# Optimization experiments

Measured on AMD Instinct MI355X. Metric: run time of the kernel, lower is better.

## Reference

```python
import jax, jax.numpy as jnp
import numpy as np


def _ste_sign(x):
    # sign with straight-through (identity) gradient, matching gradient_override_map({'Sign': 'Identity'})
    return x + jax.lax.stop_gradient(jnp.sign(x) - x)


def _ternarize(W):
    # threshold = 0.7 * mean(|W|)
    t = 0.7 * jnp.mean(jnp.abs(W))
    # alpha = mean of |W| over entries with |W| strictly beyond threshold
    pos = jnp.where(W > t, W, jnp.zeros_like(W))
    neg = jnp.where(W < -t, W, jnp.zeros_like(W))
    a = jnp.abs(pos + neg)
    n = jnp.sum(jnp.where(a > 0, jnp.ones_like(a), jnp.zeros_like(a)))
    alpha = jnp.sum(a) / n
    # ternary weights in {-1, 0, +1}: sign(sign(W+t) + sign(W-t))
    Wq = _ste_sign(_ste_sign(W + t) + _ste_sign(W - t))
    return alpha * Wq


def setup_inputs() -> dict:
    key = jax.random.key(0)
    kx, kw = jax.random.split(key)
    x = jax.random.normal(kx, (32, 56, 56, 256), dtype=jnp.float32)      # NHWC
    W = jax.random.normal(kw, (3, 3, 256, 256), dtype=jnp.float32) * 0.02  # HWIO, stddev=0.02 init
    b = jnp.zeros((256,), dtype=jnp.float32)
    return {"x": x, "W": W, "b": b}


def reference(x, W, b):
    Wq = _ternarize(W)
    y = jax.lax.conv_general_dilated(
        x, Wq,
        window_strides=(1, 1),
        padding='SAME',
        dimension_numbers=('NHWC', 'HWIO', 'NHWC'),
    )
    return y + b  # act = identity
```

## Files before the change

kernel.cpp:

```cpp
#include <hip/hip_runtime.h>
#include <hip/hip_bf16.h>
#include <stdint.h>


typedef __attribute__((ext_vector_type(8))) short short8;
typedef __attribute__((ext_vector_type(4))) float floatx4;

#define NW_ELEMS 589824
#define K_TOTAL 2304
#define PR_OFF 0
#define QV_OFF 2560
#define QC_OFF 5120
#define WQT_OFF 8192
#define XPAD_OFF 1187840
#define RED_BLOCKS 288
#define PAD_BLOCKS 13456

__device__ __forceinline__ void async16(const void* g, void* l) {
  __builtin_amdgcn_global_load_lds(
      (const __attribute__((address_space(1))) void*)g,
      (__attribute__((address_space(3))) void*)l, 16, 0, 0);
}

__device__ __forceinline__ ushort f2bf(float f) {
  __hip_bfloat16 h = __float2bfloat16(f);
  return *reinterpret_cast<ushort*>(&h);
}

__global__ __launch_bounds__(256) void pad_sumabs_kernel(
    const float* __restrict__ x, ushort* __restrict__ xpad,
    const float* __restrict__ W, double* __restrict__ pr) {
  if (blockIdx.x < RED_BLOCKS) {
    __shared__ double sds[4];
    double v = 0.0;
#pragma unroll
    for (int j = 0; j < 8; j++) {
      uint i = (blockIdx.x * 8 + j) * 256 + threadIdx.x;
      v += (double)fabsf(W[i]);
    }
#pragma unroll
    for (int off = 32; off; off >>= 1) v += __shfl_down(v, off);
    if ((threadIdx.x & 63) == 0) sds[threadIdx.x >> 6] = v;
    __syncthreads();
    if (threadIdx.x == 0) pr[blockIdx.x] = sds[0] + sds[1] + sds[2] + sds[3];
    return;
  }
  uint idx = (blockIdx.x - RED_BLOCKS) * 256 + threadIdx.x;
  uint c8 = idx & 31;
  uint sp = idx >> 5;
  uint ww = sp % 58;
  uint t = sp / 58;
  uint hh = t % 58;
  uint n = t / 58;
  ushort* dst = xpad + ((size_t)sp * 256 + c8 * 8);
  if (hh == 0 || hh == 57 || ww == 0 || ww == 57) {
    uint4 z = {0, 0, 0, 0};
    *(uint4*)dst = z;
  } else {
    const float* src = x + (((size_t)(n * 56 + (hh - 1)) * 56 + (ww - 1)) * 256 + c8 * 8);
    float4 f0 = *(const float4*)src;
    float4 f1 = *(const float4*)(src + 4);
    ushort u[8];
    u[0] = f2bf(f0.x); u[1] = f2bf(f0.y); u[2] = f2bf(f0.z); u[3] = f2bf(f0.w);
    u[4] = f2bf(f1.x); u[5] = f2bf(f1.y); u[6] = f2bf(f1.z); u[7] = f2bf(f1.w);
    *(uint4*)dst = *(uint4*)u;
  }
}

__global__ __launch_bounds__(256) void quant_kernel(
    const float* __restrict__ W, ushort* __restrict__ WqT,
    const double* __restrict__ pr, double* __restrict__ qv,
    unsigned long long* __restrict__ qc) {
  __shared__ double sds[4];
  __shared__ unsigned long long cds[4];
  double p = pr[threadIdx.x];
  if (threadIdx.x < 32) p += pr[256 + threadIdx.x];
#pragma unroll
  for (int off = 32; off; off >>= 1) p += __shfl_down(p, off);
  if ((threadIdx.x & 63) == 0) sds[threadIdx.x >> 6] = p;
  __syncthreads();
  double s = sds[0] + sds[1] + sds[2] + sds[3];
  float t = (float)(0.7 * (s / (double)NW_ELEMS));
  __syncthreads();

  double v = 0.0;
  unsigned long long cnt = 0;
  ushort u[8];
#pragma unroll
  for (int j = 0; j < 8; j++) {
    uint i = (blockIdx.x * 8 + j) * 256 + threadIdx.x;
    float w = W[i];
    bool pos = (w > t), neg = (w < -t);
    u[j] = pos ? (ushort)0x3F80 : (neg ? (ushort)0xBF80 : (ushort)0);
    if (pos || neg) { v += (double)fabsf(w); cnt++; }
  }
  *(uint4*)(WqT + (size_t)threadIdx.x * K_TOTAL + blockIdx.x * 8) = *(uint4*)u;
#pragma unroll
  for (int off = 32; off; off >>= 1) {
    v += __shfl_down(v, off);
    cnt += __shfl_down(cnt, off);
  }
  if ((threadIdx.x & 63) == 0) { sds[threadIdx.x >> 6] = v; cds[threadIdx.x >> 6] = cnt; }
  __syncthreads();
  if (threadIdx.x == 0) {
    qv[blockIdx.x] = sds[0] + sds[1] + sds[2] + sds[3];
    qc[blockIdx.x] = cds[0] + cds[1] + cds[2] + cds[3];
  }
}

__global__ __launch_bounds__(256, 2) void conv_kernel(
    const ushort* __restrict__ xpad, const ushort* __restrict__ WqT,
    const double* __restrict__ qv, const unsigned long long* __restrict__ qc,
    const float* __restrict__ bias, float* __restrict__ out) {
  __shared__ __attribute__((aligned(16))) ushort Alds[128 * 64];
  __shared__ __attribute__((aligned(16))) ushort Blds[128 * 64];
  __shared__ double ads[4];
  __shared__ double acs[4];
  uint tid = threadIdx.x;
  uint bm = blockIdx.x >> 1, bn = blockIdx.x & 1;

  uint chunk = tid & 7;
  uint rbase = tid >> 3;
  uint ceff = chunk ^ (rbase & 7);
  const ushort* asrc[4];
  const ushort* bsrc[4];
#pragma unroll
  for (int i = 0; i < 4; i++) {
    uint row = i * 32 + rbase;
    uint gm = bm * 128 + row;
    uint n = gm / 3136;
    uint rem = gm - n * 3136;
    uint h = rem / 56;
    uint w = rem - h * 56;
    asrc[i] = xpad + (((size_t)(n * 58 + h) * 58 + w) * 256 + ceff * 8);
    bsrc[i] = WqT + ((size_t)(bn * 128 + row) * K_TOTAL + ceff * 8);
  }

  floatx4 acc[4][4];
#pragma unroll
  for (int mt = 0; mt < 4; mt++)
#pragma unroll
    for (int nt = 0; nt < 4; nt++) acc[mt][nt] = (floatx4){0.f, 0.f, 0.f, 0.f};

  uint lane = tid & 63;
  uint wv = tid >> 6;
  uint wm = wv >> 1, wn = wv & 1;
  uint fr = lane & 15, fq = lane >> 4;
  uint a_row = (wm * 64 + fr) * 128;
  uint b_row = (wn * 64 + fr) * 128;
  uint swz = (fr & 7) * 16;

  for (int ks = 0; ks < 36; ks++) {
    uint kcq = (uint)ks / 9;
    uint tap = (uint)ks - kcq * 9;
    uint ky = tap / 3;
    uint kx = tap - ky * 3;
    uint aoffe = (ky * 58 + kx) * 256 + kcq * 64;
    uint boffe = tap * 256 + kcq * 64;

    __syncthreads();
#pragma unroll
    for (int i = 0; i < 4; i++)
      async16(asrc[i] + aoffe, (char*)Alds + i * 4096 + tid * 16);
#pragma unroll
    for (int i = 0; i < 4; i++)
      async16(bsrc[i] + boffe, (char*)Blds + i * 4096 + tid * 16);
    __syncthreads();

#pragma unroll
    for (int kk = 0; kk < 2; kk++) {
      uint csl = ((uint)(kk * 64) + fq * 16) ^ swz;
      short8 af[4], bfr[4];
#pragma unroll
      for (int mt = 0; mt < 4; mt++)
        af[mt] = *(const short8*)((const char*)Alds + a_row + mt * 2048 + csl);
#pragma unroll
      for (int nt = 0; nt < 4; nt++)
        bfr[nt] = *(const short8*)((const char*)Blds + b_row + nt * 2048 + csl);
#pragma unroll
      for (int mt = 0; mt < 4; mt++)
#pragma unroll
        for (int nt = 0; nt < 4; nt++)
          acc[mt][nt] = __builtin_amdgcn_mfma_f32_16x16x32_bf16(
              af[mt], bfr[nt], acc[mt][nt], 0, 0, 0);
    }
  }

  double av = qv[tid];
  double ac = (double)qc[tid];
  if (tid < 32) { av += qv[256 + tid]; ac += (double)qc[256 + tid]; }
#pragma unroll
  for (int off = 32; off; off >>= 1) {
    av += __shfl_down(av, off);
    ac += __shfl_down(ac, off);
  }
  if ((tid & 63) == 0) { ads[tid >> 6] = av; acs[tid >> 6] = ac; }
  __syncthreads();
  float alpha = (float)((ads[0] + ads[1] + ads[2] + ads[3]) /
                        (acs[0] + acs[1] + acs[2] + acs[3]));

#pragma unroll
  for (int mt = 0; mt < 4; mt++) {
    uint mb = bm * 128 + wm * 64 + mt * 16 + fq * 4;
#pragma unroll
    for (int r = 0; r < 4; r++) {
      float* orow = out + (size_t)(mb + r) * 256;
#pragma unroll
      for (int nt = 0; nt < 4; nt++) {
        uint n = bn * 128 + wn * 64 + nt * 16 + fr;
        orow[n] = acc[mt][nt][r] * alpha + bias[n];
      }
    }
  }
}

extern "C" void kernel_launch(void* const* d_in, const int* in_sizes, int n_in,
                              void* d_out, int out_size, void* d_ws, size_t ws_size,
                              hipStream_t stream) {
  const float* x = (const float*)d_in[0];
  const float* W = (const float*)d_in[1];
  const float* b = (const float*)d_in[2];
  float* out = (float*)d_out;

  double* pr = (double*)((char*)d_ws + PR_OFF);
  double* qv = (double*)((char*)d_ws + QV_OFF);
  unsigned long long* qc = (unsigned long long*)((char*)d_ws + QC_OFF);
  ushort* WqT = (ushort*)((char*)d_ws + WQT_OFF);
  ushort* xpad = (ushort*)((char*)d_ws + XPAD_OFF);

  pad_sumabs_kernel<<<RED_BLOCKS + PAD_BLOCKS, 256, 0, stream>>>(x, xpad, W, pr);
  quant_kernel<<<RED_BLOCKS, 256, 0, stream>>>(W, WqT, pr, qv, qc);
  conv_kernel<<<1568, 256, 0, stream>>>(xpad, WqT, qv, qc, b, out);
}
```

Baseline: 294.0 us.

## Fuse padding and bf16 conversion of input into conv kernel A-tile loads

Removes the separate pass that pads the input and writes a bf16 copy. The conv kernel now reads fp32 activations directly, does bounds checks for the halo, converts to bf16 in registers and stores the A tile into LDS with ordinary stores instead of async global-to-LDS loads. This saves a full write and read of the padded activation tensor. In exchange, each activation is read as fp32 (twice the bytes), is re-read and re-converted by every N-block and tap, and the synchronous loads may stall the MFMA loop.

```diff
diff --git a/kernel.cpp b/kernel.cpp
--- a/kernel.cpp
+++ b/kernel.cpp
@@ -12,9 +12,7 @@
 #define QV_OFF 2560
 #define QC_OFF 5120
 #define WQT_OFF 8192
-#define XPAD_OFF 1187840
 #define RED_BLOCKS 288
-#define PAD_BLOCKS 13456
 
 __device__ __forceinline__ void async16(const void* g, void* l) {
   __builtin_amdgcn_global_load_lds(
@@ -27,44 +25,20 @@
   return *reinterpret_cast<ushort*>(&h);
 }
 
-__global__ __launch_bounds__(256) void pad_sumabs_kernel(
-    const float* __restrict__ x, ushort* __restrict__ xpad,
+__global__ __launch_bounds__(256) void sumabs_kernel(
     const float* __restrict__ W, double* __restrict__ pr) {
-  if (blockIdx.x < RED_BLOCKS) {
-    __shared__ double sds[4];
-    double v = 0.0;
-#pragma unroll
-    for (int j = 0; j < 8; j++) {
-      uint i = (blockIdx.x * 8 + j) * 256 + threadIdx.x;
-      v += (double)fabsf(W[i]);
-    }
-#pragma unroll
-    for (int off = 32; off; off >>= 1) v += __shfl_down(v, off);
-    if ((threadIdx.x & 63) == 0) sds[threadIdx.x >> 6] = v;
-    __syncthreads();
-    if (threadIdx.x == 0) pr[blockIdx.x] = sds[0] + sds[1] + sds[2] + sds[3];
-    return;
-  }
-  uint idx = (blockIdx.x - RED_BLOCKS) * 256 + threadIdx.x;
-  uint c8 = idx & 31;
-  uint sp = idx >> 5;
-  uint ww = sp % 58;
-  uint t = sp / 58;
-  uint hh = t % 58;
-  uint n = t / 58;
-  ushort* dst = xpad + ((size_t)sp * 256 + c8 * 8);
-  if (hh == 0 || hh == 57 || ww == 0 || ww == 57) {
-    uint4 z = {0, 0, 0, 0};
-    *(uint4*)dst = z;
-  } else {
-    const float* src = x + (((size_t)(n * 56 + (hh - 1)) * 56 + (ww - 1)) * 256 + c8 * 8);
-    float4 f0 = *(const float4*)src;
-    float4 f1 = *(const float4*)(src + 4);
-    ushort u[8];
-    u[0] = f2bf(f0.x); u[1] = f2bf(f0.y); u[2] = f2bf(f0.z); u[3] = f2bf(f0.w);
-    u[4] = f2bf(f1.x); u[5] = f2bf(f1.y); u[6] = f2bf(f1.z); u[7] = f2bf(f1.w);
-    *(uint4*)dst = *(uint4*)u;
-  }
+  __shared__ double sds[4];
+  double v = 0.0;
+#pragma unroll
+  for (int j = 0; j < 8; j++) {
+    uint i = (blockIdx.x * 8 + j) * 256 + threadIdx.x;
+    v += (double)fabsf(W[i]);
+  }
+#pragma unroll
+  for (int off = 32; off; off >>= 1) v += __shfl_down(v, off);
+  if ((threadIdx.x & 63) == 0) sds[threadIdx.x >> 6] = v;
+  __syncthreads();
+  if (threadIdx.x == 0) pr[blockIdx.x] = sds[0] + sds[1] + sds[2] + sds[3];
 }
 
 __global__ __launch_bounds__(256) void quant_kernel(
@@ -109,7 +83,7 @@
 }
 
 __global__ __launch_bounds__(256, 2) void conv_kernel(
-    const ushort* __restrict__ xpad, const ushort* __restrict__ WqT,
+    const float* __restrict__ x, const ushort* __restrict__ WqT,
     const double* __restrict__ qv, const unsigned long long* __restrict__ qc,
     const float* __restrict__ bias, float* __restrict__ out) {
   __shared__ __attribute__((aligned(16))) ushort Alds[128 * 64];
@@ -122,7 +96,8 @@
   uint chunk = tid & 7;
   uint rbase = tid >> 3;
   uint ceff = chunk ^ (rbase & 7);
-  const ushort* asrc[4];
+  int hh[4], ww[4];
+  int abase[4];
   const ushort* bsrc[4];
 #pragma unroll
   for (int i = 0; i < 4; i++) {
@@ -132,7 +107,9 @@
     uint rem = gm - n * 3136;
     uint h = rem / 56;
     uint w = rem - h * 56;
-    asrc[i] = xpad + (((size_t)(n * 58 + h) * 58 + w) * 256 + ceff * 8);
+    hh[i] = (int)h;
+    ww[i] = (int)w;
+    abase[i] = (((int)n * 56 + (int)h - 1) * 56 + (int)w - 1) * 256 + (int)(ceff * 8);
     bsrc[i] = WqT + ((size_t)(bn * 128 + row) * K_TOTAL + ceff * 8);
   }
 
@@ -153,18 +130,31 @@
   for (int ks = 0; ks < 36; ks++) {
     uint kcq = (uint)ks / 9;
     uint tap = (uint)ks - kcq * 9;
-    uint ky = tap / 3;
-    uint kx = tap - ky * 3;
-    uint aoffe = (ky * 58 + kx) * 256 + kcq * 64;
+    int ky = (int)(tap / 3);
+    int kx = (int)(tap - ky * 3);
+    int aoffe = (ky * 56 + kx) * 256 + (int)(kcq * 64);
     uint boffe = tap * 256 + kcq * 64;
 
     __syncthreads();
-#pragma unroll
-    for (int i = 0; i < 4; i++)
-      async16(asrc[i] + aoffe, (char*)Alds + i * 4096 + tid * 16);
 #pragma unroll
     for (int i = 0; i < 4; i++)
       async16(bsrc[i] + boffe, (char*)Blds + i * 4096 + tid * 16);
+#pragma unroll
+    for (int i = 0; i < 4; i++) {
+      int ih = hh[i] + ky - 1;
+      int iw = ww[i] + kx - 1;
+      bool valid = ((uint)ih < 56u) && ((uint)iw < 56u);
+      float4 f0 = {0.f, 0.f, 0.f, 0.f}, f1 = {0.f, 0.f, 0.f, 0.f};
+      if (valid) {
+        const float* p = x + (abase[i] + aoffe);
+        f0 = *(const float4*)p;
+        f1 = *(const float4*)(p + 4);
+      }
+      ushort u[8];
+      u[0] = f2bf(f0.x); u[1] = f2bf(f0.y); u[2] = f2bf(f0.z); u[3] = f2bf(f0.w);
+      u[4] = f2bf(f1.x); u[5] = f2bf(f1.y); u[6] = f2bf(f1.z); u[7] = f2bf(f1.w);
+      *(uint4*)((char*)Alds + i * 4096 + tid * 16) = *(uint4*)u;
+    }
     __syncthreads();
 
 #pragma unroll
@@ -226,9 +216,8 @@
   double* qv = (double*)((char*)d_ws + QV_OFF);
   unsigned long long* qc = (unsigned long long*)((char*)d_ws + QC_OFF);
   ushort* WqT = (ushort*)((char*)d_ws + WQT_OFF);
-  ushort* xpad = (ushort*)((char*)d_ws + XPAD_OFF);
-
-  pad_sumabs_kernel<<<RED_BLOCKS + PAD_BLOCKS, 256, 0, stream>>>(x, xpad, W, pr);
+
+  sumabs_kernel<<<RED_BLOCKS, 256, 0, stream>>>(W, pr);
   quant_kernel<<<RED_BLOCKS, 256, 0, stream>>>(W, WqT, pr, qv, qc);
-  conv_kernel<<<1568, 256, 0, stream>>>(xpad, WqT, qv, qc, b, out);
-}
+  conv_kernel<<<1568, 256, 0, stream>>>(x, WqT, qv, qc, b, out);
+}
```

Result: slower. 342.6 us (+16.5%).
